# Performance work log

Measured on AMD Instinct MI355X. Metric: run time of the kernel, lower is better.

Reference implementation:

```python
import jax, jax.numpy as jnp
import numpy as np

K_BINS, EMB_WIDTH = 2048, 64
N, T = 8, 8192

def setup_inputs() -> dict:
    key = jax.random.key(0)
    k1, k2 = jax.random.split(key)
    x = jax.random.normal(k1, (N, EMB_WIDTH, T), dtype=jnp.float32)
    mask = jnp.ones((N, 1, T), dtype=jnp.float32)
    k = jax.random.normal(k2, (K_BINS, EMB_WIDTH), dtype=jnp.float32)
    return {"x": x, "mask": mask, "k": k}

def reference(x, mask, k):
    # Faithful forward of BottleneckBlock.forward with update_k=False and
    # codebook `k` already initialized (init path is a stateful randperm init).
    n, c, t = x.shape
    w = k.shape[1]
    # preprocess: [N, W, T] -> [N*T, W]
    xf = jnp.transpose(x, (0, 2, 1)).reshape(-1, c)
    mf = jnp.transpose(mask, (0, 2, 1)).reshape(-1, 1)
    prenorm = jnp.linalg.norm(xf - jnp.mean(xf)) / np.sqrt(float(xf.size))
    dist = (jnp.sum(xf * xf, axis=-1, keepdims=True)
            - 2.0 * (xf @ k.T)
            + jnp.sum(k * k, axis=-1)[None, :])  # [N*T, k_bins]
    x_l = jnp.argmin(dist, axis=-1)              # [N*T]
    fit = jax.lax.stop_gradient(jnp.mean(jnp.min(dist, axis=-1)))
    x_d = jax.lax.stop_gradient(k[x_l])          # dequantize, no_grad in torch
    # commit loss: mask is 0/1, so masked-row norm^2 == sum(mask * diff^2)
    diff2 = jnp.sum((x_d - xf) ** 2, axis=-1, keepdims=True)
    commit_loss = jnp.sum(mf * diff2) / (jnp.sum(mf) * w)
    # straight-through estimator + mask
    x_d = (xf + jax.lax.stop_gradient(x_d - xf)) * mf
    # postprocess: back to [N, W, T] and [N, T]
    x_d = jnp.transpose(x_d.reshape(n, t, w), (0, 2, 1))
    x_l = x_l.reshape(n, t)
    return x_l, x_d, commit_loss, fit, prenorm
```

## Files before the change

### kernel.cpp

```cpp
#include <hip/hip_runtime.h>

#define T_DIM 8192
#define N_DIM 8
#define C_DIM 64
#define KB    2048
#define NT    (N_DIM * T_DIM)
#define TOTX  ((size_t)NT * C_DIM)
#define NBLK  2048
#define LISTCAP 65536
#define TAU   0.045f

#define SCR_COUNT 0
#define SCR_LIST  16
#define SCR_PART  65792
#define SCR_KK    82432
#define SCR_K     90112
#define SCR_FIX   262144
#define WS_NEED_BYTES ((size_t)1310720 * 4)

typedef _Float16 half_t;
typedef _Float16 f16x8 __attribute__((ext_vector_type(8)));
typedef float    f32x16 __attribute__((ext_vector_type(16)));

__device__ __forceinline__ float np_sumsq64(const float* __restrict__ a) {
    float r[8];
    #pragma unroll
    for (int j = 0; j < 8; ++j) r[j] = __fmul_rn(a[j], a[j]);
    #pragma unroll
    for (int i = 8; i < 64; i += 8)
        #pragma unroll
        for (int j = 0; j < 8; ++j)
            r[j] = __fadd_rn(r[j], __fmul_rn(a[i + j], a[i + j]));
    return __fadd_rn(__fadd_rn(__fadd_rn(r[0], r[1]), __fadd_rn(r[2], r[3])),
                     __fadd_rn(__fadd_rn(r[4], r[5]), __fadd_rn(r[6], r[7])));
}

__global__ __launch_bounds__(64) void kprep_kernel(const float* __restrict__ k,
                                                   float* __restrict__ base) {
    const int bin = blockIdx.x * 64 + threadIdx.x;
    if (bin == 0) ((int*)base)[SCR_COUNT] = 0;

    float kv[64];
    #pragma unroll
    for (int i = 0; i < 16; ++i)
        *(float4*)&kv[i * 4] = *(const float4*)(k + (size_t)bin * 64 + i * 4);

    float kn = 0.f;
    #pragma unroll
    for (int c = 0; c < 64; ++c) kn = fmaf(kv[c], kv[c], kn);
    base[SCR_KK + bin] = np_sumsq64(kv);

    f16x8* kscr = (f16x8*)(base + SCR_K);
    const int ch = bin >> 7, b127 = bin & 127;
    #pragma unroll
    for (int slot = 0; slot < 8; ++slot) {
        f16x8 h8;
        #pragma unroll
        for (int e = 0; e < 8; ++e)
            h8[e] = (half_t)(-2.f * (float)((half_t)kv[slot * 8 + e]));
        kscr[(size_t)ch * 1152 + slot * 128 + b127] = h8;
    }
    {
        half_t knh = (half_t)kn;
        half_t knl = (half_t)(kn - (float)knh);
        f16x8 k8;
        #pragma unroll
        for (int e = 0; e < 8; ++e) k8[e] = (half_t)0.f;
        k8[0] = knh; k8[1] = knl;
        kscr[(size_t)ch * 1152 + 1024 + b127] = k8;
    }
}

__global__ __launch_bounds__(256, 2) void argmin_kernel(const float* __restrict__ x,
                                                        const float* __restrict__ mask,
                                                        float* __restrict__ out,
                                                        float* __restrict__ base) {
    __shared__ __align__(16) f16x8 xhi_s[256];
    __shared__ float psx[8][32], psxx[8][32];
    __shared__ float wres[4][32][3];

    const int tid = threadIdx.x;
    const int l   = tid & 63, w = tid >> 6;
    const int col = l & 31, kg = l >> 5;
    const int r0  = blockIdx.x * 32;
    const int n   = r0 >> 13;
    const int t0  = r0 & (T_DIM - 1);

    {
        const int row = tid & 31, slot = tid >> 5;
        float sx = 0.f, sxx = 0.f;
        f16x8 h8;
        #pragma unroll
        for (int e = 0; e < 8; ++e) {
            float v = x[((size_t)n * C_DIM + slot * 8 + e) * T_DIM + t0 + row];
            h8[e] = (half_t)v;
            sx += v; sxx = fmaf(v, v, sxx);
        }
        xhi_s[slot * 32 + row] = h8;
        psx[slot][row]  = sx;
        psxx[slot][row] = sxx;
    }
    __syncthreads();

    f16x8 a0 = xhi_s[(0 + kg) * 32 + col];
    f16x8 a1 = xhi_s[(2 + kg) * 32 + col];
    f16x8 a2 = xhi_s[(4 + kg) * 32 + col];
    f16x8 a3 = xhi_s[(6 + kg) * 32 + col];
    f16x8 aones;
    #pragma unroll
    for (int e = 0; e < 8; ++e) aones[e] = (half_t)0.f;
    if (kg == 0) { aones[0] = (half_t)1.f; aones[1] = (half_t)1.f; }

    const f16x8* kf0 = (const f16x8*)(base + SCR_K) + (size_t)w * 4 * 1152 + col;
    const int kgo = kg * 128;

    f32x16 zacc;
    #pragma unroll
    for (int r = 0; r < 16; ++r) zacc[r] = 0.f;

    float bv0 = __builtin_inff(), b20 = __builtin_inff();
    float bv1 = __builtin_inff(), b21 = __builtin_inff();
    float bv2 = __builtin_inff(), b22 = __builtin_inff();
    float bv3 = __builtin_inff(), b23 = __builtin_inff();

    f16x8 bA[4], bB[4], b4A, b4B;

#define LOADT(t, BH, B4)                                            \
    {                                                               \
        const f16x8* p = kf0 + (((t) >> 2) * 1152 + ((t) & 3) * 32);\
        BH[0] = p[kgo]; BH[1] = p[kgo + 256];                       \
        BH[2] = p[kgo + 512]; BH[3] = p[kgo + 768];                 \
        B4 = p[1024];                                               \
    }

#define UPD(J, RR, CODE)                                                     \
    {                                                                        \
        float spf = __uint_as_float(                                         \
            (__float_as_uint(acc[RR]) & 0xFFFFFFC0u) | (unsigned)(CODE));    \
        float nb2;                                                           \
        asm("v_med3_f32 %0, %1, %2, %3"                                      \
            : "=v"(nb2) : "v"(spf), "v"(bv##J), "v"(b2##J));                 \
        b2##J = nb2;                                                         \
        bv##J = fminf(bv##J, spf);                                           \
    }

#define COMPT(t, BH, B4)                                                     \
    {                                                                        \
        f32x16 acc = __builtin_amdgcn_mfma_f32_32x32x16_f16(B4, aones, zacc, 0, 0, 0); \
        acc = __builtin_amdgcn_mfma_f32_32x32x16_f16(BH[0], a0, acc, 0, 0, 0); \
        acc = __builtin_amdgcn_mfma_f32_32x32x16_f16(BH[1], a1, acc, 0, 0, 0); \
        acc = __builtin_amdgcn_mfma_f32_32x32x16_f16(BH[2], a2, acc, 0, 0, 0); \
        acc = __builtin_amdgcn_mfma_f32_32x32x16_f16(BH[3], a3, acc, 0, 0, 0); \
        const int cb4 = (t) * 4;                                             \
        UPD(0, 0, cb4 + 0)  UPD(0, 1, cb4 + 1)  UPD(0, 2, cb4 + 2)  UPD(0, 3, cb4 + 3) \
        UPD(1, 4, cb4 + 0)  UPD(1, 5, cb4 + 1)  UPD(1, 6, cb4 + 2)  UPD(1, 7, cb4 + 3) \
        UPD(2, 8, cb4 + 0)  UPD(2, 9, cb4 + 1)  UPD(2, 10, cb4 + 2) UPD(2, 11, cb4 + 3) \
        UPD(3, 12, cb4 + 0) UPD(3, 13, cb4 + 1) UPD(3, 14, cb4 + 2) UPD(3, 15, cb4 + 3) \
    }

    LOADT(0, bA, b4A);
    #pragma unroll 1
    for (int t = 0; t < 14; t += 2) {
        LOADT(t + 1, bB, b4B);
        COMPT(t, bA, b4A);
        LOADT(t + 2, bA, b4A);
        COMPT(t + 1, bB, b4B);
    }
    LOADT(15, bB, b4B);
    COMPT(14, bA, b4A);
    COMPT(15, bB, b4B);
#undef LOADT
#undef COMPT
#undef UPD

    const int bbase = w * 512 + 4 * kg;
    int c0, c1, c2, c3;
    {
        unsigned q;
        q = __float_as_uint(bv0) & 63u; c0 = bbase + (int)(q >> 2) * 32 + 0  + (int)(q & 3);
        q = __float_as_uint(bv1) & 63u; c1 = bbase + (int)(q >> 2) * 32 + 8  + (int)(q & 3);
        q = __float_as_uint(bv2) & 63u; c2 = bbase + (int)(q >> 2) * 32 + 16 + (int)(q & 3);
        q = __float_as_uint(bv3) & 63u; c3 = bbase + (int)(q >> 2) * 32 + 24 + (int)(q & 3);
    }

    float bv, b2; int bb;
    {
        float m01v; int m01c; float m01s;
        if (bv1 < bv0 || (bv1 == bv0 && c1 < c0)) { m01v = bv1; m01c = c1; }
        else                                      { m01v = bv0; m01c = c0; }
        m01s = fminf(fminf(b20, b21), fmaxf(bv0, bv1));
        float m23v; int m23c; float m23s;
        if (bv3 < bv2 || (bv3 == bv2 && c3 < c2)) { m23v = bv3; m23c = c3; }
        else                                      { m23v = bv2; m23c = c2; }
        m23s = fminf(fminf(b22, b23), fmaxf(bv2, bv3));
        if (m23v < m01v || (m23v == m01v && m23c < m01c)) { bv = m23v; bb = m23c; }
        else                                              { bv = m01v; bb = m01c; }
        b2 = fminf(fminf(m01s, m23s), fmaxf(m01v, m23v));
    }

    {
        float ov = __shfl_xor(bv, 32, 64);
        float o2 = __shfl_xor(b2, 32, 64);
        int   ob = __shfl_xor(bb, 32, 64);
        b2 = fminf(fminf(b2, o2), fmaxf(bv, ov));
        if (ov < bv || (ov == bv && ob < bb)) { bv = ov; bb = ob; }
    }

    if (kg == 0) {
        wres[w][col][0] = bv;
        wres[w][col][1] = b2;
        wres[w][col][2] = __int_as_float(bb);
    }
    __syncthreads();

    if (tid < 32) {
        const int row = tid;
        const float v0 = wres[0][row][0], v1 = wres[1][row][0];
        const float v2 = wres[2][row][0], v3 = wres[3][row][0];
        float fbv = v0; int fbb = __float_as_int(wres[0][row][2]);
        if (v1 < fbv) { fbv = v1; fbb = __float_as_int(wres[1][row][2]); }
        if (v2 < fbv) { fbv = v2; fbb = __float_as_int(wres[2][row][2]); }
        if (v3 < fbv) { fbv = v3; fbb = __float_as_int(wres[3][row][2]); }
        const float m01 = fminf(v0, v1), M01 = fmaxf(v0, v1);
        const float m23 = fminf(v2, v3), M23 = fmaxf(v2, v3);
        const float sec = fminf(fmaxf(m01, m23), fminf(M01, M23));
        const float fb2 = fminf(sec,
            fminf(fminf(wres[0][row][1], wres[1][row][1]),
                  fminf(wres[2][row][1], wres[3][row][1])));

        out[r0 + row] = (float)fbb;
        if (fb2 - fbv < TAU) {
            int idx = atomicAdd((int*)base + SCR_COUNT, 1);
            if (idx < LISTCAP) ((int*)base + SCR_LIST)[idx] = r0 + row;
        }
        float sx = 0.f, sxx = 0.f;
        #pragma unroll
        for (int sp = 0; sp < 8; ++sp) { sx += psx[sp][row]; sxx += psxx[sp][row]; }
        const float m  = mask[r0 + row];
        const float d2 = sxx + fbv;
        float vals[5] = { m * d2, d2, m, sx, sxx };
        #pragma unroll
        for (int off = 1; off <= 16; off <<= 1)
            #pragma unroll
            for (int q = 0; q < 5; ++q) vals[q] += __shfl_xor(vals[q], off, 64);
        if (tid == 0) {
            float* partials = base + SCR_PART;
            #pragma unroll
            for (int q = 0; q < 5; ++q)
                partials[(size_t)blockIdx.x * 8 + q] = vals[q];
        }
    }
}

__global__ __launch_bounds__(256) void fixup_kernel(const float* __restrict__ x,
                                                    const float* __restrict__ k,
                                                    float* __restrict__ base) {
    __shared__ float xs[32][65];
    __shared__ float sxx_s[32];
    __shared__ float redv[256];
    __shared__ int   redb[256];

    const int tid = threadIdx.x;
    const int* count    = (const int*)base + SCR_COUNT;
    const int* flaglist = (const int*)base + SCR_LIST;
    const float* kk     = base + SCR_KK;
    float* fix          = base + SCR_FIX;
    int cnt = *count;
    if (cnt > LISTCAP) cnt = LISTCAP;
    const int nb8 = ((cnt + 31) >> 5) << 3;

    const int rloc = tid & 31, part = tid >> 5;

    for (int wk = blockIdx.x; wk < nb8; wk += gridDim.x) {
        const int bi = wk >> 3, chunk = wk & 7;
        int li = bi * 32 + rloc;
        if (li >= cnt) li = bi * 32;
        const int row = flaglist[li];
        const int n = row >> 13, t = row & (T_DIM - 1);
        #pragma unroll
        for (int e = 0; e < 8; ++e)
            xs[rloc][part * 8 + e] = x[((size_t)n * C_DIM + part * 8 + e) * T_DIM + t];
        __syncthreads();
        if (tid < 32) sxx_s[tid] = np_sumsq64(&xs[tid][0]);
        __syncthreads();

        float xr[64];
        #pragma unroll
        for (int c = 0; c < 64; ++c) xr[c] = xs[rloc][c];
        const float xx = sxx_s[rloc];

        float bv = __builtin_inff();
        int   bb = 0x7fffffff;
        const int bbase = chunk * 256 + part * 32;
        #pragma unroll 1
        for (int i = 0; i < 32; i += 2) {
            const int b0 = bbase + i;
            const int b1 = b0 + 1;
            const float* k0 = k + (size_t)b0 * 64;
            const float* k1 = k + (size_t)b1 * 64;
            float d0 = 0.f, d1 = 0.f;
            #pragma unroll
            for (int c = 0; c < 64; ++c) {
                d0 = fmaf(xr[c], k0[c], d0);
                d1 = fmaf(xr[c], k1[c], d1);
            }
            float s0 = __fadd_rn(__fsub_rn(xx, __fadd_rn(d0, d0)), kk[b0]);
            float s1 = __fadd_rn(__fsub_rn(xx, __fadd_rn(d1, d1)), kk[b1]);
            if (s0 < bv || (s0 == bv && b0 < bb)) { bv = s0; bb = b0; }
            if (s1 < bv || (s1 == bv && b1 < bb)) { bv = s1; bb = b1; }
        }
        redv[tid] = bv; redb[tid] = bb;
        __syncthreads();
        if (tid < 32) {
            float fv = redv[tid]; int fb = redb[tid];
            #pragma unroll
            for (int p = 1; p < 8; ++p) {
                float ov = redv[p * 32 + tid];
                int   ob = redb[p * 32 + tid];
                if (ov < fv || (ov == fv && ob < fb)) { fv = ov; fb = ob; }
            }
            const int fi = bi * 32 + tid;
            if (fi < cnt) {
                fix[(size_t)fi * 16 + chunk * 2]     = fv;
                fix[(size_t)fi * 16 + chunk * 2 + 1] = __int_as_float(fb);
            }
        }
        __syncthreads();
    }
}

__global__ __launch_bounds__(256) void fixmerge_kernel(float* __restrict__ out,
                                                       float* __restrict__ base) {
    const int* count    = (const int*)base + SCR_COUNT;
    const int* flaglist = (const int*)base + SCR_LIST;
    const float* fix    = base + SCR_FIX;
    const int tid = threadIdx.x;
    int cnt = *count;
    if (cnt > LISTCAP) cnt = LISTCAP;

    for (int fi = blockIdx.x * 256 + tid; fi < cnt; fi += gridDim.x * 256) {
        const float* p = fix + (size_t)fi * 16;
        float bv = p[0];
        int   bb = __float_as_int(p[1]);
        #pragma unroll
        for (int c = 1; c < 8; ++c) {
            float v = p[c * 2];
            int   b = __float_as_int(p[c * 2 + 1]);
            if (v < bv || (v == bv && b < bb)) { bv = v; bb = b; }
        }
        out[flaglist[fi]] = (float)bb;
    }

    if (blockIdx.x == 0) {
        const float* partials = base + SCR_PART;
        double vals[5] = {0, 0, 0, 0, 0};
        for (int i = tid; i < NBLK; i += 256)
            #pragma unroll
            for (int q = 0; q < 5; ++q) vals[q] += (double)partials[(size_t)i * 8 + q];
        #pragma unroll
        for (int off = 1; off <= 32; off <<= 1)
            #pragma unroll
            for (int q = 0; q < 5; ++q) vals[q] += __shfl_xor(vals[q], off, 64);
        __shared__ double sred[4][5];
        const int wid = tid >> 6, lane = tid & 63;
        if (lane == 0)
            for (int q = 0; q < 5; ++q) sred[wid][q] = vals[q];
        __syncthreads();
        if (tid == 0) {
            double cm  = sred[0][0] + sred[1][0] + sred[2][0] + sred[3][0];
            double fs  = sred[0][1] + sred[1][1] + sred[2][1] + sred[3][1];
            double ms  = sred[0][2] + sred[1][2] + sred[2][2] + sred[3][2];
            double sx  = sred[0][3] + sred[1][3] + sred[2][3] + sred[3][3];
            double sxx = sred[0][4] + sred[1][4] + sred[2][4] + sred[3][4];
            double sz  = (double)TOTX;
            out[NT + TOTX + 0] = (float)(cm / (ms * (double)C_DIM));
            out[NT + TOTX + 1] = (float)(fs / (double)NT);
            out[NT + TOTX + 2] = (float)sqrt(fmax(0.0, (sxx - sx * sx / sz) / sz));
        }
    }
}

__global__ __launch_bounds__(256) void xd_kernel(const float* __restrict__ mask,
                                                 const float* __restrict__ k,
                                                 float* __restrict__ out) {
    const int row = blockIdx.x * 256 + threadIdx.x;
    const int n = row >> 13, t = row & (T_DIM - 1);
    const int b = (int)out[row];
    const float m = mask[row];
    const float* kr = k + (size_t)b * C_DIM;
    float* xd = out + NT;
    #pragma unroll
    for (int c = 0; c < C_DIM; ++c)
        xd[((size_t)n * C_DIM + c) * T_DIM + t] = kr[c] * m;
}

extern "C" void kernel_launch(void* const* d_in, const int* in_sizes, int n_in,
                              void* d_out, int out_size, void* d_ws, size_t ws_size,
                              hipStream_t stream) {
    (void)in_sizes; (void)n_in; (void)out_size;
    const float* x    = (const float*)d_in[0];
    const float* mask = (const float*)d_in[1];
    const float* k    = (const float*)d_in[2];
    float* out = (float*)d_out;
    float* base = (ws_size >= WS_NEED_BYTES) ? (float*)d_ws : out + NT;

    kprep_kernel<<<32, 64, 0, stream>>>(k, base);
    argmin_kernel<<<NBLK, 256, 0, stream>>>(x, mask, out, base);
    fixup_kernel<<<2048, 256, 0, stream>>>(x, k, base);
    fixmerge_kernel<<<256, 256, 0, stream>>>(out, base);
    xd_kernel<<<NT / 256, 256, 0, stream>>>(mask, k, out);
}
```

Before: 81.85 us.

## Process 64 rows per block to reuse codebook fragments across two MFMA tiles

Each block now handles 64 rows instead of 32, with two sets of A fragments (low and high halves). Every loaded codebook fragment feeds two MFMA chains, which halves codebook traffic per row and halves the grid size. In exchange, register pressure rises from the doubled accumulator and best/second-best state, which may hurt occupancy at the launch-bounds setting of 2 blocks per SM. The reductions and shared buffers are resized to match.

```diff
diff --git a/kernel.cpp b/kernel.cpp
--- a/kernel.cpp
+++ b/kernel.cpp
@@ -6,7 +6,7 @@
 #define KB    2048
 #define NT    (N_DIM * T_DIM)
 #define TOTX  ((size_t)NT * C_DIM)
-#define NBLK  2048
+#define NBLK  1024
 #define LISTCAP 65536
 #define TAU   0.045f
 
@@ -75,37 +75,45 @@
                                                         const float* __restrict__ mask,
                                                         float* __restrict__ out,
                                                         float* __restrict__ base) {
-    __shared__ __align__(16) f16x8 xhi_s[256];
-    __shared__ float psx[8][32], psxx[8][32];
-    __shared__ float wres[4][32][3];
+    __shared__ __align__(16) f16x8 xhi_s[512];
+    __shared__ float psx[4][64], psxx[4][64];
+    __shared__ float wres[4][64][3];
 
     const int tid = threadIdx.x;
     const int l   = tid & 63, w = tid >> 6;
     const int col = l & 31, kg = l >> 5;
-    const int r0  = blockIdx.x * 32;
+    const int r0  = blockIdx.x * 64;
     const int n   = r0 >> 13;
     const int t0  = r0 & (T_DIM - 1);
 
     {
-        const int row = tid & 31, slot = tid >> 5;
+        const int row = tid & 63, sp = tid >> 6;
         float sx = 0.f, sxx = 0.f;
-        f16x8 h8;
-        #pragma unroll
-        for (int e = 0; e < 8; ++e) {
-            float v = x[((size_t)n * C_DIM + slot * 8 + e) * T_DIM + t0 + row];
-            h8[e] = (half_t)v;
-            sx += v; sxx = fmaf(v, v, sxx);
-        }
-        xhi_s[slot * 32 + row] = h8;
-        psx[slot][row]  = sx;
-        psxx[slot][row] = sxx;
+        #pragma unroll
+        for (int ss = 0; ss < 2; ++ss) {
+            const int slot = sp * 2 + ss;
+            f16x8 h8;
+            #pragma unroll
+            for (int e = 0; e < 8; ++e) {
+                float v = x[((size_t)n * C_DIM + slot * 8 + e) * T_DIM + t0 + row];
+                h8[e] = (half_t)v;
+                sx += v; sxx = fmaf(v, v, sxx);
+            }
+            xhi_s[slot * 64 + row] = h8;
+        }
+        psx[sp][row]  = sx;
+        psxx[sp][row] = sxx;
     }
     __syncthreads();
 
-    f16x8 a0 = xhi_s[(0 + kg) * 32 + col];
-    f16x8 a1 = xhi_s[(2 + kg) * 32 + col];
-    f16x8 a2 = xhi_s[(4 + kg) * 32 + col];
-    f16x8 a3 = xhi_s[(6 + kg) * 32 + col];
+    f16x8 aL0 = xhi_s[(0 + kg) * 64 + col];
+    f16x8 aL1 = xhi_s[(2 + kg) * 64 + col];
+    f16x8 aL2 = xhi_s[(4 + kg) * 64 + col];
+    f16x8 aL3 = xhi_s[(6 + kg) * 64 + col];
+    f16x8 aH0 = xhi_s[(0 + kg) * 64 + 32 + col];
+    f16x8 aH1 = xhi_s[(2 + kg) * 64 + 32 + col];
+    f16x8 aH2 = xhi_s[(4 + kg) * 64 + 32 + col];
+    f16x8 aH3 = xhi_s[(6 + kg) * 64 + 32 + col];
     f16x8 aones;
     #pragma unroll
     for (int e = 0; e < 8; ++e) aones[e] = (half_t)0.f;
@@ -118,10 +126,14 @@
     #pragma unroll
     for (int r = 0; r < 16; ++r) zacc[r] = 0.f;
 
-    float bv0 = __builtin_inff(), b20 = __builtin_inff();
-    float bv1 = __builtin_inff(), b21 = __builtin_inff();
-    float bv2 = __builtin_inff(), b22 = __builtin_inff();
-    float bv3 = __builtin_inff(), b23 = __builtin_inff();
+    float bvL0 = __builtin_inff(), b2L0 = __builtin_inff();
+    float bvL1 = __builtin_inff(), b2L1 = __builtin_inff();
+    float bvL2 = __builtin_inff(), b2L2 = __builtin_inff();
+    float bvL3 = __builtin_inff(), b2L3 = __builtin_inff();
+    float bvH0 = __builtin_inff(), b2H0 = __builtin_inff();
+    float bvH1 = __builtin_inff(), b2H1 = __builtin_inff();
+    float bvH2 = __builtin_inff(), b2H2 = __builtin_inff();
+    float bvH3 = __builtin_inff(), b2H3 = __builtin_inff();
 
     f16x8 bA[4], bB[4], b4A, b4B;
 
@@ -133,30 +145,34 @@
         B4 = p[1024];                                               \
     }
 
-#define UPD(J, RR, CODE)                                                     \
+#define UPD(S, J, RR, CODE)                                                  \
     {                                                                        \
         float spf = __uint_as_float(                                         \
             (__float_as_uint(acc[RR]) & 0xFFFFFFC0u) | (unsigned)(CODE));    \
         float nb2;                                                           \
         asm("v_med3_f32 %0, %1, %2, %3"                                      \
-            : "=v"(nb2) : "v"(spf), "v"(bv##J), "v"(b2##J));                 \
-        b2##J = nb2;                                                         \
-        bv##J = fminf(bv##J, spf);                                           \
-    }
-
-#define COMPT(t, BH, B4)                                                     \
+            : "=v"(nb2) : "v"(spf), "v"(bv##S##J), "v"(b2##S##J));           \
+        b2##S##J = nb2;                                                      \
+        bv##S##J = fminf(bv##S##J, spf);                                     \
+    }
+
+#define COMPS(S, A0, A1, A2, A3, t, BH, B4)                                  \
     {                                                                        \
         f32x16 acc = __builtin_amdgcn_mfma_f32_32x32x16_f16(B4, aones, zacc, 0, 0, 0); \
-        acc = __builtin_amdgcn_mfma_f32_32x32x16_f16(BH[0], a0, acc, 0, 0, 0); \
-        acc = __builtin_amdgcn_mfma_f32_32x32x16_f16(BH[1], a1, acc, 0, 0, 0); \
-        acc = __builtin_amdgcn_mfma_f32_32x32x16_f16(BH[2], a2, acc, 0, 0, 0); \
-        acc = __builtin_amdgcn_mfma_f32_32x32x16_f16(BH[3], a3, acc, 0, 0, 0); \
+        acc = __builtin_amdgcn_mfma_f32_32x32x16_f16(BH[0], A0, acc, 0, 0, 0); \
+        acc = __builtin_amdgcn_mfma_f32_32x32x16_f16(BH[1], A1, acc, 0, 0, 0); \
+        acc = __builtin_amdgcn_mfma_f32_32x32x16_f16(BH[2], A2, acc, 0, 0, 0); \
+        acc = __builtin_amdgcn_mfma_f32_32x32x16_f16(BH[3], A3, acc, 0, 0, 0); \
         const int cb4 = (t) * 4;                                             \
-        UPD(0, 0, cb4 + 0)  UPD(0, 1, cb4 + 1)  UPD(0, 2, cb4 + 2)  UPD(0, 3, cb4 + 3) \
-        UPD(1, 4, cb4 + 0)  UPD(1, 5, cb4 + 1)  UPD(1, 6, cb4 + 2)  UPD(1, 7, cb4 + 3) \
-        UPD(2, 8, cb4 + 0)  UPD(2, 9, cb4 + 1)  UPD(2, 10, cb4 + 2) UPD(2, 11, cb4 + 3) \
-        UPD(3, 12, cb4 + 0) UPD(3, 13, cb4 + 1) UPD(3, 14, cb4 + 2) UPD(3, 15, cb4 + 3) \
-    }
+        UPD(S, 0, 0, cb4 + 0)  UPD(S, 0, 1, cb4 + 1)  UPD(S, 0, 2, cb4 + 2)  UPD(S, 0, 3, cb4 + 3) \
+        UPD(S, 1, 4, cb4 + 0)  UPD(S, 1, 5, cb4 + 1)  UPD(S, 1, 6, cb4 + 2)  UPD(S, 1, 7, cb4 + 3) \
+        UPD(S, 2, 8, cb4 + 0)  UPD(S, 2, 9, cb4 + 1)  UPD(S, 2, 10, cb4 + 2) UPD(S, 2, 11, cb4 + 3) \
+        UPD(S, 3, 12, cb4 + 0) UPD(S, 3, 13, cb4 + 1) UPD(S, 3, 14, cb4 + 2) UPD(S, 3, 15, cb4 + 3) \
+    }
+
+#define COMPT(t, BH, B4)                                                     \
+    COMPS(L, aL0, aL1, aL2, aL3, t, BH, B4)                                  \
+    COMPS(H, aH0, aH1, aH2, aH3, t, BH, B4)
 
     LOADT(0, bA, b4A);
     #pragma unroll 1
@@ -171,49 +187,53 @@
     COMPT(15, bB, b4B);
 #undef LOADT
 #undef COMPT
+#undef COMPS
 #undef UPD
 
     const int bbase = w * 512 + 4 * kg;
-    int c0, c1, c2, c3;
-    {
+    #pragma unroll
+    for (int s = 0; s < 2; ++s) {
+        float v0 = s ? bvH0 : bvL0, s0 = s ? b2H0 : b2L0;
+        float v1 = s ? bvH1 : bvL1, s1 = s ? b2H1 : b2L1;
+        float v2 = s ? bvH2 : bvL2, s2 = s ? b2H2 : b2L2;
+        float v3 = s ? bvH3 : bvL3, s3 = s ? b2H3 : b2L3;
         unsigned q;
-        q = __float_as_uint(bv0) & 63u; c0 = bbase + (int)(q >> 2) * 32 + 0  + (int)(q & 3);
-        q = __float_as_uint(bv1) & 63u; c1 = bbase + (int)(q >> 2) * 32 + 8  + (int)(q & 3);
-        q = __float_as_uint(bv2) & 63u; c2 = bbase + (int)(q >> 2) * 32 + 16 + (int)(q & 3);
-        q = __float_as_uint(bv3) & 63u; c3 = bbase + (int)(q >> 2) * 32 + 24 + (int)(q & 3);
-    }
-
-    float bv, b2; int bb;
-    {
-        float m01v; int m01c; float m01s;
-        if (bv1 < bv0 || (bv1 == bv0 && c1 < c0)) { m01v = bv1; m01c = c1; }
-        else                                      { m01v = bv0; m01c = c0; }
-        m01s = fminf(fminf(b20, b21), fmaxf(bv0, bv1));
-        float m23v; int m23c; float m23s;
-        if (bv3 < bv2 || (bv3 == bv2 && c3 < c2)) { m23v = bv3; m23c = c3; }
-        else                                      { m23v = bv2; m23c = c2; }
-        m23s = fminf(fminf(b22, b23), fmaxf(bv2, bv3));
-        if (m23v < m01v || (m23v == m01v && m23c < m01c)) { bv = m23v; bb = m23c; }
-        else                                              { bv = m01v; bb = m01c; }
-        b2 = fminf(fminf(m01s, m23s), fmaxf(m01v, m23v));
-    }
-
-    {
-        float ov = __shfl_xor(bv, 32, 64);
-        float o2 = __shfl_xor(b2, 32, 64);
-        int   ob = __shfl_xor(bb, 32, 64);
-        b2 = fminf(fminf(b2, o2), fmaxf(bv, ov));
-        if (ov < bv || (ov == bv && ob < bb)) { bv = ov; bb = ob; }
-    }
-
-    if (kg == 0) {
-        wres[w][col][0] = bv;
-        wres[w][col][1] = b2;
-        wres[w][col][2] = __int_as_float(bb);
+        int c0, c1, c2, c3;
+        q = __float_as_uint(v0) & 63u; c0 = bbase + (int)(q >> 2) * 32 + 0  + (int)(q & 3);
+        q = __float_as_uint(v1) & 63u; c1 = bbase + (int)(q >> 2) * 32 + 8  + (int)(q & 3);
+        q = __float_as_uint(v2) & 63u; c2 = bbase + (int)(q >> 2) * 32 + 16 + (int)(q & 3);
+        q = __float_as_uint(v3) & 63u; c3 = bbase + (int)(q >> 2) * 32 + 24 + (int)(q & 3);
+
+        float bv, b2; int bb;
+        {
+            float m01v; int m01c; float m01s;
+            if (v1 < v0 || (v1 == v0 && c1 < c0)) { m01v = v1; m01c = c1; }
+            else                                  { m01v = v0; m01c = c0; }
+            m01s = fminf(fminf(s0, s1), fmaxf(v0, v1));
+            float m23v; int m23c; float m23s;
+            if (v3 < v2 || (v3 == v2 && c3 < c2)) { m23v = v3; m23c = c3; }
+            else                                  { m23v = v2; m23c = c2; }
+            m23s = fminf(fminf(s2, s3), fmaxf(v2, v3));
+            if (m23v < m01v || (m23v == m01v && m23c < m01c)) { bv = m23v; bb = m23c; }
+            else                                              { bv = m01v; bb = m01c; }
+            b2 = fminf(fminf(m01s, m23s), fmaxf(m01v, m23v));
+        }
+        {
+            float ov = __shfl_xor(bv, 32, 64);
+            float o2 = __shfl_xor(b2, 32, 64);
+            int   ob = __shfl_xor(bb, 32, 64);
+            b2 = fminf(fminf(b2, o2), fmaxf(bv, ov));
+            if (ov < bv || (ov == bv && ob < bb)) { bv = ov; bb = ob; }
+        }
+        if (kg == 0) {
+            wres[w][s * 32 + col][0] = bv;
+            wres[w][s * 32 + col][1] = b2;
+            wres[w][s * 32 + col][2] = __int_as_float(bb);
+        }
     }
     __syncthreads();
 
-    if (tid < 32) {
+    if (tid < 64) {
         const int row = tid;
         const float v0 = wres[0][row][0], v1 = wres[1][row][0];
         const float v2 = wres[2][row][0], v3 = wres[3][row][0];
@@ -235,12 +255,12 @@
         }
         float sx = 0.f, sxx = 0.f;
         #pragma unroll
-        for (int sp = 0; sp < 8; ++sp) { sx += psx[sp][row]; sxx += psxx[sp][row]; }
+        for (int sp = 0; sp < 4; ++sp) { sx += psx[sp][row]; sxx += psxx[sp][row]; }
         const float m  = mask[r0 + row];
         const float d2 = sxx + fbv;
         float vals[5] = { m * d2, d2, m, sx, sxx };
         #pragma unroll
-        for (int off = 1; off <= 16; off <<= 1)
+        for (int off = 1; off <= 32; off <<= 1)
             #pragma unroll
             for (int q = 0; q < 5; ++q) vals[q] += __shfl_xor(vals[q], off, 64);
         if (tid == 0) {
```

Result: faster. 77.99 us (-4.7%).
